# Optimization experiments

Measured on AMD Instinct MI355X. Metric: run time of the kernel, lower is better.

## Reference

```python
import jax, jax.numpy as jnp
import numpy as np

U, N, C, D, E, K, NS = 100000, 50000, 20, 128, 1000000, 50000, 9


def setup_inputs() -> dict:
    key = jax.random.key(0)
    ks = jax.random.split(key, 13)
    s = 0.1  # embedding init scale
    return {
        "user_emb": jax.random.normal(ks[0], (U, D), jnp.float32) * s,
        "news_emb": jax.random.normal(ks[1], (N, D), jnp.float32) * s,
        "cat_emb": jax.random.normal(ks[2], (C, D), jnp.float32) * s,
        "cx": jax.random.normal(ks[3], (U, D), jnp.float32) * s,
        "W_ih": jax.random.normal(ks[4], (4 * D, D), jnp.float32) * (1.0 / np.sqrt(D)),
        "W_hh": jax.random.normal(ks[5], (4 * D, D), jnp.float32) * (1.0 / np.sqrt(D)),
        "b_ih": jax.random.normal(ks[6], (4 * D,), jnp.float32) * (1.0 / np.sqrt(D)),
        "b_hh": jax.random.normal(ks[7], (4 * D,), jnp.float32) * (1.0 / np.sqrt(D)),
        "edge_src": jax.random.randint(ks[8], (E,), 0, N, jnp.int32),
        "edge_dst": jax.random.randint(ks[9], (E,), 0, U, jnp.int32),
        "edge_cat": jax.random.randint(ks[10], (E,), 0, C, jnp.int32),
        "ns_idx": jax.random.randint(ks[11], (K, NS), 0, N, jnp.int32),
        "user_score_idx": jax.random.randint(ks[12], (K,), 0, U, jnp.int32),
    }


def reference(user_emb, news_emb, cat_emb, cx, W_ih, W_hh, b_ih, b_hh,
              edge_src, edge_dst, edge_cat, ns_idx, user_score_idx):
    # --- GCN message passing (DGL send_and_recv on 'clicked_reverse': news -> user) ---
    # per-edge message: src news embedding * category (edge) embedding
    msg = news_emb[edge_src] * cat_emb[edge_cat]                      # [E, D]
    agg = jax.ops.segment_sum(msg, edge_dst, num_segments=U)          # [U, D]
    cnt = jax.ops.segment_sum(jnp.ones_like(msg[:, 0]), edge_dst, num_segments=U)
    mean_msg = agg / jnp.maximum(cnt, 1.0)[:, None]                   # mailbox mean
    x = user_emb + mean_msg                                           # residual add -> LSTM input

    # --- LSTMCell (PyTorch gate order i, f, g, o), prev h = original user_emb ---
    gates = x @ W_ih.T + b_ih + user_emb @ W_hh.T + b_hh              # [U, 4D]
    i, f, g, o = jnp.split(gates, 4, axis=-1)
    c_new = jax.nn.sigmoid(f) * cx + jax.nn.sigmoid(i) * jnp.tanh(g)
    h_new = jax.nn.sigmoid(o) * jnp.tanh(c_new)                       # updated user node_emb

    # --- candidate scoring: (user * news_cand).sum(-1) over 9 candidates ---
    cand_u = h_new[user_score_idx]                                    # [K, D]
    cand_n = news_emb[ns_idx]                                         # [K, 9, D]
    score = jnp.einsum('kd,knd->kn', cand_u, cand_n)                  # [K, 9]
    return score
```

## Files before the change

kernel.cpp:

```cpp
#include <hip/hip_runtime.h>
#include <math.h>

#define U_CNT 100000
#define N_CNT 50000
#define C_CNT 20
#define D_DIM 128
#define E_CNT 1000000
#define K_CNT 50000
#define NS_CNT 9
#define CAP 64

#define BM 64
#define NBLK 1563

#define OFF_CNT    0
#define OFF_BPT    400384
#define OFF_BSUM   662528
#define OFF_NBF    665600
#define OFF_BUCKET 13465600
#define OFF_ABF    39065664

typedef __attribute__((ext_vector_type(8))) short bf16x8;
typedef __attribute__((ext_vector_type(4))) float f32x4;

__device__ __forceinline__ unsigned short f2bf(float f) {
    unsigned u = __builtin_bit_cast(unsigned, f);
    u = (u + 0x7FFF + ((u >> 16) & 1)) >> 16;
    return (unsigned short)u;
}
__device__ __forceinline__ float bf2f(unsigned short b) {
    return __builtin_bit_cast(float, (unsigned)b << 16);
}

__device__ __forceinline__ void gload16(const void* g, void* l) {
    __builtin_amdgcn_global_load_lds(
        (const __attribute__((address_space(1))) unsigned int*)g,
        (__attribute__((address_space(3))) unsigned int*)l, 16, 0, 0);
}

__global__ void k_zero(int* __restrict__ cnt) {
    int i = blockIdx.x * 256 + threadIdx.x;
    if (i < U_CNT) cnt[i] = 0;
}

__global__ void k_prep(const float* __restrict__ Wih, const float* __restrict__ Whh,
                       const float* __restrict__ bih, const float* __restrict__ bhh,
                       unsigned short* __restrict__ Bpt, float* __restrict__ bsum_p) {
    int idx = blockIdx.x * 256 + threadIdx.x;
    if (idx < 512) {
        int dim = idx >> 2, g = idx & 3;
        bsum_p[idx] = bih[g * 128 + dim] + bhh[g * 128 + dim];
    }
    if (idx >= 512 * 256) return;
    int col = idx >> 8, kp = idx & 255;
    int seg = kp >> 6, gst = (kp >> 3) & 7, e = kp & 7;
    int k = seg * 64 + (gst ^ (col & 7)) * 8 + e;
    int d = col >> 2, g = col & 3;
    int j = g * 128 + d;
    float v = (k < 128) ? Wih[j * 128 + k] : Whh[j * 128 + (k - 128)];
    Bpt[idx] = f2bf(v);
}

__global__ void k_nbf(const float* __restrict__ news, unsigned short* __restrict__ nbf) {
    int i = blockIdx.x * 256 + threadIdx.x;
    if (i >= N_CNT * 32) return;
    float4 v = ((const float4*)news)[i];
    ushort4 o = {f2bf(v.x), f2bf(v.y), f2bf(v.z), f2bf(v.w)};
    ((ushort4*)nbf)[i] = o;
}

__global__ void k_bucket(const int* __restrict__ dst, const int* __restrict__ esrc,
                         const int* __restrict__ ecat, int* __restrict__ cnt,
                         int* __restrict__ bucket) {
    int e = blockIdx.x * 256 + threadIdx.x;
    if (e >= E_CNT) return;
    int d = dst[e];
    int slot = atomicAdd(&cnt[d], 1);
    if (slot < CAP) bucket[d * CAP + slot] = (esrc[e] & 0xFFFF) | (ecat[e] << 16);
}

__global__ void k_agg(const float* __restrict__ user_emb,
                      const unsigned short* __restrict__ news_bf,
                      const float* __restrict__ cat_emb,
                      const int* __restrict__ cnt,
                      const int* __restrict__ bucket,
                      unsigned short* __restrict__ Abf) {
    int wid  = (blockIdx.x * blockDim.x + threadIdx.x) >> 6;
    int lane = threadIdx.x & 63;
    if (wid >= U_CNT) return;
    int deg = cnt[wid];
    if (deg > CAP) deg = CAP;
    int half = lane >> 5, lid = lane & 31;
    const int* bp = bucket + wid * CAP;
    float4 acc = {0.f, 0.f, 0.f, 0.f};
    int trips = (deg + 1) >> 1;
    int p = 0; float vmask = 0.f;
    if (trips > 0) {
        int e0 = half;
        p = bp[e0 < deg ? e0 : 0];
        vmask = (e0 < deg) ? 1.f : 0.f;
    }
    for (int t = 0; t < trips; ++t) {
        int en = 2 * (t + 1) + half;
        int pn = 0; float vn = 0.f;
        if (t + 1 < trips) {
            pn = bp[en < deg ? en : 0];
            vn = (en < deg) ? 1.f : 0.f;
        }
        int s = p & 0xFFFF;
        int c = p >> 16;
        ushort4 nv = *(const ushort4*)&news_bf[(size_t)s * 128 + lid * 4];
        float4  cv = *(const float4*)&cat_emb[c * 128 + lid * 4];
        acc.x += vmask * bf2f(nv.x) * cv.x;
        acc.y += vmask * bf2f(nv.y) * cv.y;
        acc.z += vmask * bf2f(nv.z) * cv.z;
        acc.w += vmask * bf2f(nv.w) * cv.w;
        p = pn; vmask = vn;
    }
    acc.x += __shfl_xor(acc.x, 32, 64);
    acc.y += __shfl_xor(acc.y, 32, 64);
    acc.z += __shfl_xor(acc.z, 32, 64);
    acc.w += __shfl_xor(acc.w, 32, 64);
    if (half == 0) {
        float inv = 1.0f / (float)(deg < 1 ? 1 : deg);
        float4 ue = *(const float4*)&user_emb[(size_t)wid * 128 + lid * 4];
        float4 xv = {ue.x + acc.x * inv, ue.y + acc.y * inv,
                     ue.z + acc.z * inv, ue.w + acc.w * inv};
        int seg = lid >> 4;
        int gr  = (lid >> 1) & 7;
        int eo  = (lid & 1) * 4;
        int pos = seg * 64 + ((gr ^ (wid & 7)) * 8) + eo;
        size_t base = (size_t)wid * 256;
        ushort4 xb = {f2bf(xv.x), f2bf(xv.y), f2bf(xv.z), f2bf(xv.w)};
        ushort4 ub = {f2bf(ue.x), f2bf(ue.y), f2bf(ue.z), f2bf(ue.w)};
        *(ushort4*)&Abf[base + pos] = xb;
        *(ushort4*)&Abf[base + 128 + pos] = ub;
    }
}

__global__ __launch_bounds__(512, 4) void k_gemm_lstm(
    const unsigned short* __restrict__ Abf, const unsigned short* __restrict__ Bpt,
    const float* __restrict__ bsum_p, const float* __restrict__ cx,
    float* __restrict__ hout)
{
    __shared__ __align__(16) char smem[8192 + 65536];
    int t = threadIdx.x, l = t & 63, w = t >> 6;
    int u0 = blockIdx.x * BM;
    int wn0 = w * 64;

    f32x4 acc[4][4];
#pragma unroll
    for (int m = 0; m < 4; ++m)
#pragma unroll
        for (int n = 0; n < 4; ++n) acc[m][n] = (f32x4){0.f, 0.f, 0.f, 0.f};

    int lhi = l >> 3, llo = l & 7;
    for (int step = 0; step < 4; ++step) {
        int k0 = step * 64;
#pragma unroll
        for (int ii = 0; ii < 9; ++ii) {
            int inst = w * 9 + ii;
            if (inst < 8) {
                int row = inst * 8 + lhi;
                gload16(Abf + (size_t)(u0 + row) * 256 + k0 + llo * 8,
                        smem + inst * 1024);
            } else {
                int b = inst - 8;
                int col = b * 8 + lhi;
                gload16(Bpt + (size_t)col * 256 + k0 + llo * 8,
                        smem + 8192 + b * 1024);
            }
        }
        asm volatile("s_waitcnt vmcnt(0)" ::: "memory");
        __syncthreads();

#pragma unroll
        for (int kf = 0; kf < 2; ++kf) {
            int swz = ((kf * 4 + (l >> 4)) ^ (l & 7)) * 16;
            bf16x8 af[4], bfr[4];
#pragma unroll
            for (int m = 0; m < 4; ++m)
                af[m] = *(const bf16x8*)(smem + (m * 16 + (l & 15)) * 128 + swz);
#pragma unroll
            for (int n = 0; n < 4; ++n)
                bfr[n] = *(const bf16x8*)(smem + 8192 + (wn0 + n * 16 + (l & 15)) * 128 + swz);
#pragma unroll
            for (int m = 0; m < 4; ++m)
#pragma unroll
                for (int n = 0; n < 4; ++n)
                    acc[m][n] = __builtin_amdgcn_mfma_f32_16x16x32_bf16(
                        af[m], bfr[n], acc[m][n], 0, 0, 0);
        }
        __syncthreads();
    }

    float* gbuf = (float*)smem;
#pragma unroll
    for (int m = 0; m < 4; ++m) {
#pragma unroll
        for (int n = 0; n < 4; ++n)
#pragma unroll
            for (int r = 0; r < 4; ++r)
                gbuf[((l >> 4) * 4 + r) * 516 + wn0 + n * 16 + (l & 15)] = acc[m][n][r];
        __syncthreads();
#pragma unroll
        for (int i = 0; i < 4; ++i) {
            int c = t + 512 * i;
            int row = c >> 7, dim = c & 127;
            int u = u0 + m * 16 + row;
            float4 gv = *(const float4*)&gbuf[row * 516 + dim * 4];
            if (u < U_CNT) {
                float4 bs = *(const float4*)&bsum_p[dim * 4];
                float I = gv.x + bs.x, F = gv.y + bs.y, G = gv.z + bs.z, O = gv.w + bs.w;
                float cxv = cx[(size_t)u * 128 + dim];
                float si = 1.f / (1.f + expf(-I));
                float sf = 1.f / (1.f + expf(-F));
                float so = 1.f / (1.f + expf(-O));
                float cn = sf * cxv + si * tanhf(G);
                hout[(size_t)u * 128 + dim] = so * tanhf(cn);
            }
        }
        __syncthreads();
    }
}

__global__ void k_score(const float* __restrict__ h, const float* __restrict__ news_emb,
                        const int* __restrict__ ns_idx, const int* __restrict__ usi,
                        float* __restrict__ out) {
    int wid  = (blockIdx.x * blockDim.x + threadIdx.x) >> 6;
    int lane = threadIdx.x & 63;
    if (wid >= K_CNT) return;
    int u = usi[wid];
    float2 hv = ((const float2*)h)[(size_t)u * 64 + lane];
    const float2* n2 = (const float2*)news_emb;
    float val = 0.f;
#pragma unroll
    for (int j = 0; j < 9; ++j) {
        int n = ns_idx[wid * 9 + j];
        float2 nv = n2[(size_t)n * 64 + lane];
        float p = hv.x * nv.x + hv.y * nv.y;
#pragma unroll
        for (int off = 32; off; off >>= 1) p += __shfl_xor(p, off, 64);
        if (lane == j) val = p;
    }
    if (lane < 9) out[wid * 9 + lane] = val;
}

extern "C" void kernel_launch(void* const* d_in, const int* in_sizes, int n_in,
                              void* d_out, int out_size, void* d_ws, size_t ws_size,
                              hipStream_t stream) {
    const float* user_emb = (const float*)d_in[0];
    const float* news_emb = (const float*)d_in[1];
    const float* cat_emb  = (const float*)d_in[2];
    const float* cx       = (const float*)d_in[3];
    const float* W_ih     = (const float*)d_in[4];
    const float* W_hh     = (const float*)d_in[5];
    const float* b_ih     = (const float*)d_in[6];
    const float* b_hh     = (const float*)d_in[7];
    const int* edge_src   = (const int*)d_in[8];
    const int* edge_dst   = (const int*)d_in[9];
    const int* edge_cat   = (const int*)d_in[10];
    const int* ns_idx     = (const int*)d_in[11];
    const int* usi        = (const int*)d_in[12];
    float* out = (float*)d_out;

    char* ws = (char*)d_ws;
    int*            cnt    = (int*)(ws + OFF_CNT);
    unsigned short* Bpt    = (unsigned short*)(ws + OFF_BPT);
    float*          bsum_p = (float*)(ws + OFF_BSUM);
    unsigned short* nbf    = (unsigned short*)(ws + OFF_NBF);
    int*            bucket = (int*)(ws + OFF_BUCKET);
    unsigned short* Abf    = (unsigned short*)(ws + OFF_ABF);
    float*          h      = (float*)(ws + OFF_ABF);

    k_zero<<<(U_CNT + 255) / 256, 256, 0, stream>>>(cnt);
    k_prep<<<512, 256, 0, stream>>>(W_ih, W_hh, b_ih, b_hh, Bpt, bsum_p);
    k_nbf<<<6250, 256, 0, stream>>>(news_emb, nbf);
    k_bucket<<<(E_CNT + 255) / 256, 256, 0, stream>>>(edge_dst, edge_src, edge_cat, cnt, bucket);
    k_agg<<<25000, 256, 0, stream>>>(user_emb, nbf, cat_emb, cnt, bucket, Abf);
    k_gemm_lstm<<<NBLK, 512, 0, stream>>>(Abf, Bpt, bsum_p, cx, h);
    k_score<<<(K_CNT * 64 + 255) / 256, 256, 0, stream>>>(h, news_emb, ns_idx, usi, out);
}
```

Measured before the change: 468.4 us.

## Double-buffer GEMM LDS staging, fast LSTM activations, bf16 hidden state and scoring

The LSTM GEMM now walks K in eight chunks of 32 with a double-buffered LDS stage. The next chunk's global-to-LDS loads are issued before the current MFMAs run, and a new swizzle replaces the old single-buffer wait-all loop. The epilogue handles 32 rows per pass and uses exp2/rcp-based sigmoid and tanh instead of expf/tanhf. The hidden state is written as bf16 in place over the A buffer, and the scoring kernel reads the bf16 hidden state and bf16 news embeddings with 32-lane groups per candidate row, halving gather traffic. Precision drops in the scores (bf16 h and news, approximate transcendentals), and the in-place h overwrite of Abf relies on row-block ownership.

```diff
diff --git a/kernel.cpp b/kernel.cpp
--- a/kernel.cpp
+++ b/kernel.cpp
@@ -30,6 +30,16 @@
 }
 __device__ __forceinline__ float bf2f(unsigned short b) {
     return __builtin_bit_cast(float, (unsigned)b << 16);
+}
+
+__device__ __forceinline__ float sig_fast(float x) {
+    float t = __builtin_amdgcn_exp2f(x * -1.44269504f);
+    return __builtin_amdgcn_rcpf(1.f + t);
+}
+__device__ __forceinline__ float tanh_fast(float x) {
+    x = fminf(fmaxf(x, -15.f), 15.f);
+    float t = __builtin_amdgcn_exp2f(x * 2.88539008f);
+    return (t - 1.f) * __builtin_amdgcn_rcpf(t + 1.f);
 }
 
 __device__ __forceinline__ void gload16(const void* g, void* l) {
@@ -138,12 +148,38 @@
     }
 }
 
+#define STAGE(K0, BUF)                                                                   \
+    {                                                                                    \
+        int bg3 = ((K0) >> 3) & 7;                                                       \
+        int seg64 = ((K0) >> 6) * 64;                                                    \
+        char* Ab_ = smem + (BUF) * 4096;                                                 \
+        char* Bb_ = smem + 8192 + (BUF) * 32768;                                         \
+        _Pragma("unroll")                                                                \
+        for (int ii = 0; ii < 5; ++ii) {                                                 \
+            int inst = w + ii * 8;                                                       \
+            if (inst < 4) {                                                              \
+                int row = inst * 16 + (l >> 2);                                          \
+                int kg = (l & 3) ^ (row & 3);                                            \
+                gload16(Abf + (size_t)(u0 + row) * 256 + seg64 +                         \
+                            ((bg3 + kg) ^ (row & 7)) * 8,                                \
+                        Ab_ + inst * 1024 + l * 16);                                     \
+            } else if (inst < 36) {                                                      \
+                int b = inst - 4;                                                        \
+                int col = b * 16 + (l >> 2);                                             \
+                int kg = (l & 3) ^ (col & 3);                                            \
+                gload16(Bpt + (size_t)col * 256 + seg64 +                                \
+                            ((bg3 + kg) ^ (col & 7)) * 8,                                \
+                        Bb_ + b * 1024 + l * 16);                                        \
+            }                                                                            \
+        }                                                                                \
+    }
+
 __global__ __launch_bounds__(512, 4) void k_gemm_lstm(
     const unsigned short* __restrict__ Abf, const unsigned short* __restrict__ Bpt,
     const float* __restrict__ bsum_p, const float* __restrict__ cx,
-    float* __restrict__ hout)
+    unsigned short* __restrict__ hout)
 {
-    __shared__ __align__(16) char smem[8192 + 65536];
+    __shared__ __align__(16) char smem[73728];
     int t = threadIdx.x, l = t & 63, w = t >> 6;
     int u0 = blockIdx.x * BM;
     int wn0 = w * 64;
@@ -154,96 +190,89 @@
 #pragma unroll
         for (int n = 0; n < 4; ++n) acc[m][n] = (f32x4){0.f, 0.f, 0.f, 0.f};
 
-    int lhi = l >> 3, llo = l & 7;
-    for (int step = 0; step < 4; ++step) {
-        int k0 = step * 64;
-#pragma unroll
-        for (int ii = 0; ii < 9; ++ii) {
-            int inst = w * 9 + ii;
-            if (inst < 8) {
-                int row = inst * 8 + lhi;
-                gload16(Abf + (size_t)(u0 + row) * 256 + k0 + llo * 8,
-                        smem + inst * 1024);
-            } else {
-                int b = inst - 8;
-                int col = b * 8 + lhi;
-                gload16(Bpt + (size_t)col * 256 + k0 + llo * 8,
-                        smem + 8192 + b * 1024);
-            }
-        }
-        asm volatile("s_waitcnt vmcnt(0)" ::: "memory");
+    STAGE(0, 0);
+    __syncthreads();
+
+#pragma unroll
+    for (int step = 0; step < 8; ++step) {
+        int cur = step & 1;
+        if (step < 7) STAGE((step + 1) * 32, cur ^ 1);
+        const char* Ab = smem + cur * 4096;
+        const char* Bb = smem + 8192 + cur * 32768;
+        int kg = l >> 4;
+        bf16x8 af[4], bfr[4];
+#pragma unroll
+        for (int m = 0; m < 4; ++m) {
+            int row = m * 16 + (l & 15);
+            af[m] = *(const bf16x8*)(Ab + row * 64 + ((kg ^ (row & 3)) * 16));
+        }
+#pragma unroll
+        for (int n = 0; n < 4; ++n) {
+            int col = wn0 + n * 16 + (l & 15);
+            bfr[n] = *(const bf16x8*)(Bb + col * 64 + ((kg ^ (col & 3)) * 16));
+        }
+#pragma unroll
+        for (int m = 0; m < 4; ++m)
+#pragma unroll
+            for (int n = 0; n < 4; ++n)
+                acc[m][n] = __builtin_amdgcn_mfma_f32_16x16x32_bf16(
+                    af[m], bfr[n], acc[m][n], 0, 0, 0);
         __syncthreads();
-
-#pragma unroll
-        for (int kf = 0; kf < 2; ++kf) {
-            int swz = ((kf * 4 + (l >> 4)) ^ (l & 7)) * 16;
-            bf16x8 af[4], bfr[4];
-#pragma unroll
-            for (int m = 0; m < 4; ++m)
-                af[m] = *(const bf16x8*)(smem + (m * 16 + (l & 15)) * 128 + swz);
+    }
+
+    float* gbuf = (float*)smem;
+#pragma unroll
+    for (int mm = 0; mm < 2; ++mm) {
+#pragma unroll
+        for (int mo = 0; mo < 2; ++mo) {
 #pragma unroll
             for (int n = 0; n < 4; ++n)
-                bfr[n] = *(const bf16x8*)(smem + 8192 + (wn0 + n * 16 + (l & 15)) * 128 + swz);
-#pragma unroll
-            for (int m = 0; m < 4; ++m)
-#pragma unroll
-                for (int n = 0; n < 4; ++n)
-                    acc[m][n] = __builtin_amdgcn_mfma_f32_16x16x32_bf16(
-                        af[m], bfr[n], acc[m][n], 0, 0, 0);
+#pragma unroll
+                for (int r = 0; r < 4; ++r)
+                    gbuf[(mo * 16 + (l >> 4) * 4 + r) * 516 + wn0 + n * 16 + (l & 15)] =
+                        acc[mm * 2 + mo][n][r];
         }
         __syncthreads();
-    }
-
-    float* gbuf = (float*)smem;
-#pragma unroll
-    for (int m = 0; m < 4; ++m) {
-#pragma unroll
-        for (int n = 0; n < 4; ++n)
-#pragma unroll
-            for (int r = 0; r < 4; ++r)
-                gbuf[((l >> 4) * 4 + r) * 516 + wn0 + n * 16 + (l & 15)] = acc[m][n][r];
-        __syncthreads();
-#pragma unroll
-        for (int i = 0; i < 4; ++i) {
+#pragma unroll
+        for (int i = 0; i < 8; ++i) {
             int c = t + 512 * i;
             int row = c >> 7, dim = c & 127;
-            int u = u0 + m * 16 + row;
-            float4 gv = *(const float4*)&gbuf[row * 516 + dim * 4];
+            int u = u0 + mm * 32 + row;
             if (u < U_CNT) {
+                float4 gv = *(const float4*)&gbuf[row * 516 + dim * 4];
                 float4 bs = *(const float4*)&bsum_p[dim * 4];
                 float I = gv.x + bs.x, F = gv.y + bs.y, G = gv.z + bs.z, O = gv.w + bs.w;
                 float cxv = cx[(size_t)u * 128 + dim];
-                float si = 1.f / (1.f + expf(-I));
-                float sf = 1.f / (1.f + expf(-F));
-                float so = 1.f / (1.f + expf(-O));
-                float cn = sf * cxv + si * tanhf(G);
-                hout[(size_t)u * 128 + dim] = so * tanhf(cn);
+                float cn = sig_fast(F) * cxv + sig_fast(I) * tanh_fast(G);
+                hout[(size_t)u * 256 + dim] = f2bf(sig_fast(O) * tanh_fast(cn));
             }
         }
         __syncthreads();
     }
 }
 
-__global__ void k_score(const float* __restrict__ h, const float* __restrict__ news_emb,
+__global__ void k_score(const unsigned short* __restrict__ hbf,
+                        const unsigned short* __restrict__ nbf,
                         const int* __restrict__ ns_idx, const int* __restrict__ usi,
                         float* __restrict__ out) {
-    int wid  = (blockIdx.x * blockDim.x + threadIdx.x) >> 6;
-    int lane = threadIdx.x & 63;
-    if (wid >= K_CNT) return;
-    int u = usi[wid];
-    float2 hv = ((const float2*)h)[(size_t)u * 64 + lane];
-    const float2* n2 = (const float2*)news_emb;
+    int gh  = (blockIdx.x * 256 + threadIdx.x) >> 5;
+    int lid = threadIdx.x & 31;
+    if (gh >= K_CNT) return;
+    int u = usi[gh];
+    ushort4 hv = *(const ushort4*)&hbf[(size_t)u * 256 + lid * 4];
+    float h0 = bf2f(hv.x), h1 = bf2f(hv.y), h2 = bf2f(hv.z), h3 = bf2f(hv.w);
+    const int* np = ns_idx + gh * 9;
     float val = 0.f;
 #pragma unroll
     for (int j = 0; j < 9; ++j) {
-        int n = ns_idx[wid * 9 + j];
-        float2 nv = n2[(size_t)n * 64 + lane];
-        float p = hv.x * nv.x + hv.y * nv.y;
-#pragma unroll
-        for (int off = 32; off; off >>= 1) p += __shfl_xor(p, off, 64);
-        if (lane == j) val = p;
-    }
-    if (lane < 9) out[wid * 9 + lane] = val;
+        int n = np[j];
+        ushort4 nv = *(const ushort4*)&nbf[(size_t)n * 128 + lid * 4];
+        float p = h0 * bf2f(nv.x) + h1 * bf2f(nv.y) + h2 * bf2f(nv.z) + h3 * bf2f(nv.w);
+#pragma unroll
+        for (int off = 16; off; off >>= 1) p += __shfl_xor(p, off, 64);
+        if (lid == j) val = p;
+    }
+    if (lid < 9) out[(size_t)gh * 9 + lid] = val;
 }
 
 extern "C" void kernel_launch(void* const* d_in, const int* in_sizes, int n_in,
@@ -271,13 +300,13 @@
     unsigned short* nbf    = (unsigned short*)(ws + OFF_NBF);
     int*            bucket = (int*)(ws + OFF_BUCKET);
     unsigned short* Abf    = (unsigned short*)(ws + OFF_ABF);
-    float*          h      = (float*)(ws + OFF_ABF);
+    unsigned short* hbf    = (unsigned short*)(ws + OFF_ABF);
 
     k_zero<<<(U_CNT + 255) / 256, 256, 0, stream>>>(cnt);
     k_prep<<<512, 256, 0, stream>>>(W_ih, W_hh, b_ih, b_hh, Bpt, bsum_p);
     k_nbf<<<6250, 256, 0, stream>>>(news_emb, nbf);
     k_bucket<<<(E_CNT + 255) / 256, 256, 0, stream>>>(edge_dst, edge_src, edge_cat, cnt, bucket);
     k_agg<<<25000, 256, 0, stream>>>(user_emb, nbf, cat_emb, cnt, bucket, Abf);
-    k_gemm_lstm<<<NBLK, 512, 0, stream>>>(Abf, Bpt, bsum_p, cx, h);
-    k_score<<<(K_CNT * 64 + 255) / 256, 256, 0, stream>>>(h, news_emb, ns_idx, usi, out);
-}
+    k_gemm_lstm<<<NBLK, 512, 0, stream>>>(Abf, Bpt, bsum_p, cx, hbf);
+    k_score<<<(K_CNT * 32 + 255) / 256, 256, 0, stream>>>(hbf, nbf, ns_idx, usi, out);
+}
```

Measured after the change: 427.3 us. 1.1x faster.
